# Kernel optimization log

Measured on AMD Instinct MI355X. Metric: run time of the kernel, lower is better.

The kernel has to match this reference:

```python
import jax, jax.numpy as jnp
import numpy as np

K = 3  # kernel_size, padding=1, stride=1 (same-size unfold)


def unfold3x3(x):
    """x: [B, C, H, W] -> [B, C, 9, H, W], matching torch.nn.Unfold(3, padding=1)
    channel-major / row-major kernel-position ordering."""
    H, W = x.shape[2], x.shape[3]
    xp = jnp.pad(x, ((0, 0), (0, 0), (1, 1), (1, 1)))
    patches = [xp[:, :, i:i + H, j:j + W] for i in range(K) for j in range(K)]
    return jnp.stack(patches, axis=2)


def setup_inputs() -> dict:
    key = jax.random.key(0)
    k1, k2, k3, k4 = jax.random.split(key, 4)
    B, CF, H, W = 2, 64, 64, 2048
    coord_C = 3
    out_Cs = (16, 64)  # out_Cs[-1] == CF
    features = jax.random.normal(k1, (B, CF, H, W), dtype=jnp.float32)
    coord = jax.random.normal(k2, (B, coord_C, H, W), dtype=jnp.float32)
    w0 = jax.random.normal(k3, (out_Cs[0], coord_C), dtype=jnp.float32) * 0.1
    w1 = jax.random.normal(k4, (out_Cs[1], out_Cs[0]), dtype=jnp.float32) * 0.1
    return {"features": features, "coord": coord, "w0": w0, "w1": w1}


def reference(features, coord, w0, w1):
    # --- gather 3x3 coord neighborhood, relative coords ---
    coord_sample = unfold3x3(coord)                    # [B, 3, 9, H, W]
    center = coord[:, :, None]                         # [B, 3, 1, H, W]
    rel = coord_sample - center
    rel = jnp.where(center == -1.0, 0.0, rel)          # zero invalid centers
    # --- weight-generation MLP: 1x1 convs over channel dim, per pixel & neighbor ---
    h = jnp.einsum('oc,bcnhw->bonhw', w0, rel)         # [B, 16, 9, H, W]
    h = jnp.einsum('oc,bcnhw->bonhw', w1, h)           # [B, 64, 9, H, W]
    weights = jax.nn.relu(h)                           # ReLU only after last layer
    # --- gather 3x3 feature neighborhood, weighted combine ---
    feat_sample = unfold3x3(features)                  # [B, CF, 9, H, W]
    out = feat_sample * weights                        # [B, CF, 9, H, W]
    B, CF, KK, H, W = out.shape
    return out.reshape(B, CF * KK, H, W)               # [B, CF*9, H, W]
```

## Files before the change

kernel.cpp:

```cpp
#include <hip/hip_runtime.h>

#define BB   2
#define CF_  64
#define CC   3
#define HH   64
#define WW   2048
#define HWs  (HH * WW)
#define KK   9
#define TPB  512

typedef float f4 __attribute__((ext_vector_type(4)));

__global__ __launch_bounds__(TPB, 4) void fused_unfold_mlp_kernel(
    const float* __restrict__ feat,
    const float* __restrict__ coord,
    const float* __restrict__ w0,
    const float* __restrict__ w1,
    float* __restrict__ out)
{
    const int t  = threadIdx.x;
    const int id = blockIdx.x;
    const int h  = id & (HH - 1);
    const int cf = (id >> 6) & (CF_ - 1);
    const int b  = id >> 12;

    float m[CC];
#pragma unroll
    for (int c = 0; c < CC; c++) {
        float acc = 0.f;
#pragma unroll
        for (int k = 0; k < 16; k++)
            acc = fmaf(w1[cf * 16 + k], w0[k * CC + c], acc);
        m[c] = __uint_as_float(__builtin_amdgcn_readfirstlane(__float_as_uint(acc)));
    }

    const int g  = t * 4;
    const int bL = (g >= 4) ? (g - 4) : 0;
    const int bR = (g + 4 <= WW - 4) ? (g + 4) : (WW - 4);
    const bool eL = (t == 0), eR = (t == TPB - 1);

    const int r0 = (h > 0      ? h - 1 : 0     ) * WW;
    const int r1 = h * WW;
    const int r2 = (h < HH - 1 ? h + 1 : HH - 1) * WW;
    const float rm0 = (h > 0)      ? 1.f : 0.f;
    const float rm2 = (h < HH - 1) ? 1.f : 0.f;

    const float* __restrict__ cb = coord + (size_t)b * CC * HWs;
    const float* __restrict__ fr = feat  + ((size_t)b * CF_ + cf) * HWs;
    float* __restrict__ ob = out + (size_t)(b * CF_ + cf) * KK * HWs
                                 + (size_t)h * WW + g;

    float mk[CC][4], bb[4];

    auto ldwin = [&](const float* base, float* w) {
        *(f4*)(w)     = *(const f4*)(base + bL);
        *(f4*)(w + 4) = *(const f4*)(base + g);
        *(f4*)(w + 8) = *(const f4*)(base + bR);
    };

    auto doRow = [&](int ro, float rm, int n0, bool isCenter) {
        float cw[CC][12], fw[12];
#pragma unroll
        for (int c = 0; c < CC; c++) ldwin(cb + (size_t)c * HWs + ro, cw[c]);
        ldwin(fr + ro, fw);

        if (isCenter) {
#pragma unroll
            for (int px = 0; px < 4; px++) {
                float acc = 0.f;
#pragma unroll
                for (int c = 0; c < CC; c++) {
                    const float cen = cw[c][4 + px];
                    const float kk  = (cen != -1.0f) ? 1.f : 0.f;
                    mk[c][px] = m[c] * kk;
                    acc = fmaf(mk[c][px], cen, acc);
                }
                bb[px] = acc;
            }
        }

#pragma unroll
        for (int j = 0; j < 3; j++) {
            f4 v;
#pragma unroll
            for (int px = 0; px < 4; px++) {
                const int idx = 4 + px + j - 1;
                float wgt = fmaf(mk[2][px], cw[2][idx],
                            fmaf(mk[1][px], cw[1][idx],
                            fmaf(mk[0][px], cw[0][idx], -bb[px])));
                float ft = fw[idx];
                if (px == 0 && j == 0) ft = eL ? 0.f : ft;
                if (px == 3 && j == 2) ft = eR ? 0.f : ft;
                v[px] = ft * rm * fmaxf(wgt, 0.f);
            }
            __builtin_nontemporal_store(v, (f4*)(ob + (size_t)(n0 + j) * HWs));
        }
    };

    doRow(r1, 1.f, 3, true);
    doRow(r0, rm0, 0, false);
    doRow(r2, rm2, 6, false);
}

extern "C" void kernel_launch(void* const* d_in, const int* in_sizes, int n_in,
                              void* d_out, int out_size, void* d_ws, size_t ws_size,
                              hipStream_t stream) {
    const float* feat  = (const float*)d_in[0];
    const float* coord = (const float*)d_in[1];
    const float* w0    = (const float*)d_in[2];
    const float* w1    = (const float*)d_in[3];
    float* out = (float*)d_out;

    const int blocks = BB * CF_ * HH;
    fused_unfold_mlp_kernel<<<blocks, TPB, 0, stream>>>(feat, coord, w0, w1, out);
}
```

Baseline: 727.8 us.

## Assign one output plane row-half per block instead of all nine offsets

Restructures the grid so each block handles a single kernel offset for one half-row, with one float4 output per thread, instead of one block producing all nine offset planes for a full row. Out-of-range rows write zeros and exit early, and the nontemporal stores become plain stores. This trades the old reuse of loaded windows across offsets for more blocks and simpler per-thread work. Coordinate and feature reads are repeated per offset, and L1/L2 have to absorb those extra reads. The output stores are now regular cached stores, which may pollute the cache on a write-dominated kernel.

```diff
diff --git a/kernel.cpp b/kernel.cpp
--- a/kernel.cpp
+++ b/kernel.cpp
@@ -7,99 +7,87 @@
 #define WW   2048
 #define HWs  (HH * WW)
 #define KK   9
-#define TPB  512
+#define NPL  (BB * CF_ * KK)
 
 typedef float f4 __attribute__((ext_vector_type(4)));
 
-__global__ __launch_bounds__(TPB, 4) void fused_unfold_mlp_kernel(
+__global__ __launch_bounds__(256) void fused_unfold_mlp_kernel(
     const float* __restrict__ feat,
     const float* __restrict__ coord,
     const float* __restrict__ w0,
     const float* __restrict__ w1,
     float* __restrict__ out)
 {
-    const int t  = threadIdx.x;
-    const int id = blockIdx.x;
-    const int h  = id & (HH - 1);
-    const int cf = (id >> 6) & (CF_ - 1);
-    const int b  = id >> 12;
+    const int t   = threadIdx.x;
+    const int bid = blockIdx.x;
+    const int whalf = bid & 1;
+    const int h     = (bid >> 1) & (HH - 1);
+    const int rest  = bid >> 7;
+    const int b     = rest >= (CF_ * KK);
+    const int pn    = rest - b * (CF_ * KK);
+    const int cf    = pn / KK;
+    const int n     = pn - cf * KK;
+    const int di    = n / 3 - 1;
+    const int dj    = n % 3 - 1;
 
-    float m[CC];
+    const int w0c = (whalf * 256 + t) * 4;
+    f4* __restrict__ ost = (f4*)(out + (size_t)rest * HWs + (size_t)h * WW + w0c);
+
+    const int hh = h + di;
+    if (hh < 0 || hh >= HH) {
+        f4 z = {0.f, 0.f, 0.f, 0.f};
+        *ost = z;
+        return;
+    }
+
+    float m0a = 0.f, m1a = 0.f, m2a = 0.f;
+#pragma unroll
+    for (int k = 0; k < 16; k++) {
+        const float a = w1[cf * 16 + k];
+        m0a = fmaf(a, w0[k * CC + 0], m0a);
+        m1a = fmaf(a, w0[k * CC + 1], m1a);
+        m2a = fmaf(a, w0[k * CC + 2], m2a);
+    }
+
+    const bool eL = (w0c == 0)      && (dj < 0);
+    const bool eR = (w0c == WW - 4) && (dj > 0);
+    const int  ws = w0c + dj + (eL ? 1 : 0) - (eR ? 1 : 0);
+
+    const float* __restrict__ cb = coord + (size_t)b * CC * HWs;
+    const float* __restrict__ fp = feat + ((size_t)b * CF_ + cf) * HWs;
+
+    f4 cen[CC], raw[CC];
 #pragma unroll
     for (int c = 0; c < CC; c++) {
-        float acc = 0.f;
+        cen[c] = *(const f4*)(cb + (size_t)c * HWs + (size_t)h  * WW + w0c);
+        raw[c] = *(const f4*)(cb + (size_t)c * HWs + (size_t)hh * WW + ws);
+    }
+    const f4 fraw = *(const f4*)(fp + (size_t)hh * WW + ws);
+
+    float s[CC][4], ft[4];
 #pragma unroll
-        for (int k = 0; k < 16; k++)
-            acc = fmaf(w1[cf * 16 + k], w0[k * CC + c], acc);
-        m[c] = __uint_as_float(__builtin_amdgcn_readfirstlane(__float_as_uint(acc)));
+    for (int px = 0; px < 4; px++) {
+#pragma unroll
+        for (int c = 0; c < CC; c++)
+            s[c][px] = eL ? (px >= 1 ? raw[c][px - 1] : 0.f)
+                     : eR ? (px <= 2 ? raw[c][px + 1] : 0.f)
+                     :      raw[c][px];
+        ft[px] = eL ? (px >= 1 ? fraw[px - 1] : 0.f)
+               : eR ? (px <= 2 ? fraw[px + 1] : 0.f)
+               :      fraw[px];
     }
 
-    const int g  = t * 4;
-    const int bL = (g >= 4) ? (g - 4) : 0;
-    const int bR = (g + 4 <= WW - 4) ? (g + 4) : (WW - 4);
-    const bool eL = (t == 0), eR = (t == TPB - 1);
-
-    const int r0 = (h > 0      ? h - 1 : 0     ) * WW;
-    const int r1 = h * WW;
-    const int r2 = (h < HH - 1 ? h + 1 : HH - 1) * WW;
-    const float rm0 = (h > 0)      ? 1.f : 0.f;
-    const float rm2 = (h < HH - 1) ? 1.f : 0.f;
-
-    const float* __restrict__ cb = coord + (size_t)b * CC * HWs;
-    const float* __restrict__ fr = feat  + ((size_t)b * CF_ + cf) * HWs;
-    float* __restrict__ ob = out + (size_t)(b * CF_ + cf) * KK * HWs
-                                 + (size_t)h * WW + g;
-
-    float mk[CC][4], bb[4];
-
-    auto ldwin = [&](const float* base, float* w) {
-        *(f4*)(w)     = *(const f4*)(base + bL);
-        *(f4*)(w + 4) = *(const f4*)(base + g);
-        *(f4*)(w + 8) = *(const f4*)(base + bR);
-    };
-
-    auto doRow = [&](int ro, float rm, int n0, bool isCenter) {
-        float cw[CC][12], fw[12];
+    f4 v;
 #pragma unroll
-        for (int c = 0; c < CC; c++) ldwin(cb + (size_t)c * HWs + ro, cw[c]);
-        ldwin(fr + ro, fw);
-
-        if (isCenter) {
-#pragma unroll
-            for (int px = 0; px < 4; px++) {
-                float acc = 0.f;
-#pragma unroll
-                for (int c = 0; c < CC; c++) {
-                    const float cen = cw[c][4 + px];
-                    const float kk  = (cen != -1.0f) ? 1.f : 0.f;
-                    mk[c][px] = m[c] * kk;
-                    acc = fmaf(mk[c][px], cen, acc);
-                }
-                bb[px] = acc;
-            }
-        }
-
-#pragma unroll
-        for (int j = 0; j < 3; j++) {
-            f4 v;
-#pragma unroll
-            for (int px = 0; px < 4; px++) {
-                const int idx = 4 + px + j - 1;
-                float wgt = fmaf(mk[2][px], cw[2][idx],
-                            fmaf(mk[1][px], cw[1][idx],
-                            fmaf(mk[0][px], cw[0][idx], -bb[px])));
-                float ft = fw[idx];
-                if (px == 0 && j == 0) ft = eL ? 0.f : ft;
-                if (px == 3 && j == 2) ft = eR ? 0.f : ft;
-                v[px] = ft * rm * fmaxf(wgt, 0.f);
-            }
-            __builtin_nontemporal_store(v, (f4*)(ob + (size_t)(n0 + j) * HWs));
-        }
-    };
-
-    doRow(r1, 1.f, 3, true);
-    doRow(r0, rm0, 0, false);
-    doRow(r2, rm2, 6, false);
+    for (int px = 0; px < 4; px++) {
+        const float k0 = (cen[0][px] != -1.f) ? m0a : 0.f;
+        const float k1 = (cen[1][px] != -1.f) ? m1a : 0.f;
+        const float k2 = (cen[2][px] != -1.f) ? m2a : 0.f;
+        const float bb = fmaf(k2, cen[2][px], fmaf(k1, cen[1][px], k0 * cen[0][px]));
+        float wgt = fmaf(k2, s[2][px], fmaf(k1, s[1][px], fmaf(k0, s[0][px], -bb)));
+        v[px] = ft[px] * fmaxf(wgt, 0.f);
+    }
+    *ost = v;
 }
 
 extern "C" void kernel_launch(void* const* d_in, const int* in_sizes, int n_in,
@@ -111,6 +99,6 @@
     const float* w1    = (const float*)d_in[3];
     float* out = (float*)d_out;
 
-    const int blocks = BB * CF_ * HH;
-    fused_unfold_mlp_kernel<<<blocks, TPB, 0, stream>>>(feat, coord, w0, w1, out);
+    const int blocks = NPL * HH * 2;
+    fused_unfold_mlp_kernel<<<blocks, 256, 0, stream>>>(feat, coord, w0, w1, out);
 }
```

New measurement: 778.7 us. 1.07x slower.
